# Optimization experiments

Measured on AMD Instinct MI355X. Metric: run time of the kernel, lower is better.

The kernel has to match this reference:

```python
import jax, jax.numpy as jnp
import numpy as np

IN_FEAT = 3 * 32 * 32  # channels*height*width
HID = 1024
CLASSES = 10
EPS = 1e-5


def binarize(w):
    # Deterministic BinaryConnect: sign(w) in {-1, +1} (sign(0) -> +1)
    return jnp.where(w >= 0, 1.0, -1.0).astype(w.dtype)


def batchnorm(h, gamma, beta):
    # training-mode BatchNorm1d: biased batch stats over batch axis
    mean = jnp.mean(h, axis=0)
    var = jnp.var(h, axis=0)
    return gamma * (h - mean) * jax.lax.rsqrt(var + EPS) + beta


def setup_inputs() -> dict:
    key = jax.random.key(0)
    ks = jax.random.split(key, 6)
    x = jax.random.normal(ks[0], (8192, 3, 32, 32), dtype=jnp.float32)
    # latent real-valued weights, torch Linear layout [out, in], kaiming-ish scale
    W1 = jax.random.normal(ks[1], (HID, IN_FEAT), dtype=jnp.float32) * (1.0 / np.sqrt(IN_FEAT))
    W2 = jax.random.normal(ks[2], (HID, HID), dtype=jnp.float32) * (1.0 / np.sqrt(HID))
    W3 = jax.random.normal(ks[3], (HID, HID), dtype=jnp.float32) * (1.0 / np.sqrt(HID))
    W4 = jax.random.normal(ks[4], (CLASSES, HID), dtype=jnp.float32) * (1.0 / np.sqrt(HID))
    g1 = jnp.ones((HID,), jnp.float32); b1 = jnp.zeros((HID,), jnp.float32)
    g2 = jnp.ones((HID,), jnp.float32); b2 = jnp.zeros((HID,), jnp.float32)
    g3 = jnp.ones((HID,), jnp.float32); b3 = jnp.zeros((HID,), jnp.float32)
    return {"x": x, "W1": W1, "W2": W2, "W3": W3, "W4": W4,
            "g1": g1, "b1": b1, "g2": g2, "b2": b2, "g3": g3, "b3": b3}


def reference(x, W1, W2, W3, W4, g1, b1, g2, b2, g3, b3):
    h = x.reshape(-1, IN_FEAT)                       # [B, 3072]
    h = jax.nn.relu(h @ binarize(W1).T)              # [B, 1024]
    h = batchnorm(h, g1, b1)
    h = jax.nn.relu(h @ binarize(W2).T)
    h = batchnorm(h, g2, b2)
    h = jax.nn.relu(h @ binarize(W3).T)
    h = batchnorm(h, g3, b3)
    return h @ binarize(W4).T                        # [B, classes]
```

## Files before the change

### kernel.cpp

```cpp
#include <hip/hip_runtime.h>
#include <stdint.h>

typedef unsigned short u16;
typedef __attribute__((ext_vector_type(8))) unsigned short ushort8;
typedef __attribute__((ext_vector_type(4))) unsigned short ushort4v;
typedef __attribute__((ext_vector_type(8))) __bf16 bf16x8;
typedef __attribute__((ext_vector_type(4))) float f32x4;

__device__ __forceinline__ u16 f2bf(float f) {
    union { float f; unsigned int u; } v; v.f = f;
    unsigned int r = v.u + 0x7FFFu + ((v.u >> 16) & 1u);
    return (u16)(r >> 16);
}
__device__ __forceinline__ float bf2f(u16 b) {
    union { unsigned int u; float f; } v; v.u = ((unsigned int)b) << 16;
    return v.f;
}

typedef __attribute__((address_space(1))) const uint32_t* gptr_t;
typedef __attribute__((address_space(3))) uint32_t* lptr_t;
__device__ __forceinline__ void async_copy16(const void* g, void* l) {
    __builtin_amdgcn_global_load_lds((gptr_t)g, (lptr_t)l, 16, 0, 0);
}


__global__ __launch_bounds__(256) void f32_to_bf16_kernel(
    const float* __restrict__ in, u16* __restrict__ out, int n8)
{
    int i = blockIdx.x * 256 + threadIdx.x;
    if (i >= n8) return;
    const float4* p = (const float4*)(in + (size_t)i * 8);
    float4 x0 = p[0], x1 = p[1];
    ushort8 o;
    o[0] = f2bf(x0.x); o[1] = f2bf(x0.y); o[2] = f2bf(x0.z); o[3] = f2bf(x0.w);
    o[4] = f2bf(x1.x); o[5] = f2bf(x1.y); o[6] = f2bf(x1.z); o[7] = f2bf(x1.w);
    *(ushort8*)(out + (size_t)i * 8) = o;
}

__global__ __launch_bounds__(256) void binarize_kernel(
    const float* __restrict__ in, u16* __restrict__ out, int n8)
{
    int i = blockIdx.x * 256 + threadIdx.x;
    if (i >= n8) return;
    const float4* p = (const float4*)(in + (size_t)i * 8);
    float4 x0 = p[0], x1 = p[1];
    ushort8 o;
    o[0] = x0.x >= 0.f ? 0x3F80 : 0xBF80;
    o[1] = x0.y >= 0.f ? 0x3F80 : 0xBF80;
    o[2] = x0.z >= 0.f ? 0x3F80 : 0xBF80;
    o[3] = x0.w >= 0.f ? 0x3F80 : 0xBF80;
    o[4] = x1.x >= 0.f ? 0x3F80 : 0xBF80;
    o[5] = x1.y >= 0.f ? 0x3F80 : 0xBF80;
    o[6] = x1.z >= 0.f ? 0x3F80 : 0xBF80;
    o[7] = x1.w >= 0.f ? 0x3F80 : 0xBF80;
    *(ushort8*)(out + (size_t)i * 8) = o;
}

__global__ __launch_bounds__(256) void build_w4t(
    const float* __restrict__ W4, u16* __restrict__ W4T)
{
    int idx = blockIdx.x * 256 + threadIdx.x;
    int k = idx >> 4, c = idx & 15;
    u16 v = 0;
    if (c < 10) v = (W4[(size_t)c * 1024 + k] >= 0.f) ? 0x3F80 : 0xBF80;
    W4T[idx] = v;
}

__global__ __launch_bounds__(256) void rescale_w(
    const float* __restrict__ W, const float* __restrict__ ss,
    u16* __restrict__ Wp, float* __restrict__ bias)
{
    const int lane = threadIdx.x & 63;
    const int wid  = threadIdx.x >> 6;
    const int r    = blockIdx.x * 4 + wid;
    float bsum = 0.f;
    #pragma unroll
    for (int k0 = 0; k0 < 1024; k0 += 256) {
        int k = k0 + lane * 4;
        float4 w  = *(const float4*)(W + (size_t)r * 1024 + k);
        float4 sc = *(const float4*)(ss + k);
        float4 sh = *(const float4*)(ss + 1024 + k);
        ushort4v o;
        o[0] = f2bf(w.x >= 0.f ? sc.x : -sc.x);
        o[1] = f2bf(w.y >= 0.f ? sc.y : -sc.y);
        o[2] = f2bf(w.z >= 0.f ? sc.z : -sc.z);
        o[3] = f2bf(w.w >= 0.f ? sc.w : -sc.w);
        bsum += (w.x >= 0.f ? sh.x : -sh.x) + (w.y >= 0.f ? sh.y : -sh.y)
              + (w.z >= 0.f ? sh.z : -sh.z) + (w.w >= 0.f ? sh.w : -sh.w);
        *(ushort4v*)(Wp + (size_t)r * 1024 + k) = o;
    }
    #pragma unroll
    for (int off = 32; off; off >>= 1) bsum += __shfl_xor(bsum, off, 64);
    if (lane == 0) bias[r] = bsum;
}


__global__ __launch_bounds__(256) void gemm_fused(
    const u16* __restrict__ A, const u16* __restrict__ B,
    u16* __restrict__ H, const float* __restrict__ bias,
    float* __restrict__ partS, float* __restrict__ partS2,
    int M, int N, int K)
{
    __shared__ __align__(16) u16 As[2][128 * 64];
    __shared__ __align__(16) u16 Bs[2][128 * 64];

    const int tid  = threadIdx.x;
    const int wid  = tid >> 6;
    const int lane = tid & 63;
    const int lr   = lane & 15;
    const int hk   = lane >> 4;
    const int x7   = lr & 7;
    const int wr   = wid >> 1;
    const int wc   = wid & 1;
    const int row0 = blockIdx.x * 128;
    const int col0 = blockIdx.y * 128;

    const int s_r = tid >> 3;
    const int s_c = (((tid & 7) ^ (s_r & 7)) << 3);
    const u16* gA = A + (size_t)(row0 + s_r) * K + s_c;
    const u16* gB = B + (size_t)(col0 + s_r) * K + s_c;

    int a_base[4], b_base[4];
    #pragma unroll
    for (int i = 0; i < 4; ++i) a_base[i] = (wr * 64 + i * 16 + lr) * 64;
    #pragma unroll
    for (int j = 0; j < 4; ++j) b_base[j] = (wc * 64 + j * 16 + lr) * 64;
    const int xs0 = ((hk)     ^ x7) << 3;
    const int xs1 = ((hk + 4) ^ x7) << 3;

    f32x4 acc[4][4];
    #pragma unroll
    for (int i = 0; i < 4; ++i)
        #pragma unroll
        for (int j = 0; j < 4; ++j)
            acc[i][j] = (f32x4){0.f, 0.f, 0.f, 0.f};

    const int NT = K >> 6;

    auto STAGE = [&](int buf, int t) {
        const u16* pa = gA + (size_t)t * 64;
        const u16* pb = gB + (size_t)t * 64;
        #pragma unroll
        for (int i = 0; i < 4; ++i)
            async_copy16(pa + (size_t)i * 32 * K, &As[buf][i * 2048 + wid * 512]);
        #pragma unroll
        for (int i = 0; i < 4; ++i)
            async_copy16(pb + (size_t)i * 32 * K, &Bs[buf][i * 2048 + wid * 512]);
    };

    STAGE(0, 0);
    STAGE(1, 1);

    for (int t = 0; t < NT; ++t) {
        const int buf = t & 1;
        if (t + 1 < NT) asm volatile("s_waitcnt vmcnt(8)" ::: "memory");
        else            asm volatile("s_waitcnt vmcnt(0)" ::: "memory");
        __builtin_amdgcn_s_barrier();

        bf16x8 af[4][2], bg[4][2];
        #pragma unroll
        for (int i = 0; i < 4; ++i) {
            af[i][0] = *(const bf16x8*)&As[buf][a_base[i] + xs0];
            af[i][1] = *(const bf16x8*)&As[buf][a_base[i] + xs1];
        }
        #pragma unroll
        for (int j = 0; j < 4; ++j) {
            bg[j][0] = *(const bf16x8*)&Bs[buf][b_base[j] + xs0];
            bg[j][1] = *(const bf16x8*)&Bs[buf][b_base[j] + xs1];
        }
        asm volatile("s_waitcnt lgkmcnt(0)" ::: "memory");
        __builtin_amdgcn_sched_barrier(0);
        __builtin_amdgcn_s_barrier();

        if (t + 2 < NT) STAGE(buf, t + 2);

        __builtin_amdgcn_s_setprio(1);
        #pragma unroll
        for (int kk = 0; kk < 2; ++kk)
            #pragma unroll
            for (int i = 0; i < 4; ++i)
                #pragma unroll
                for (int j = 0; j < 4; ++j)
                    acc[i][j] = __builtin_amdgcn_mfma_f32_16x16x32_bf16(
                        af[i][kk], bg[j][kk], acc[i][j], 0, 0, 0);
        __builtin_amdgcn_s_setprio(0);
    }

    const int er = hk * 4;
    #pragma unroll
    for (int j = 0; j < 4; ++j) {
        const int c = col0 + wc * 64 + j * 16 + lr;
        const float bj = bias ? bias[c] : 0.f;
        float s = 0.f, s2 = 0.f;
        #pragma unroll
        for (int i = 0; i < 4; ++i) {
            const int r = row0 + wr * 64 + i * 16 + er;
            #pragma unroll
            for (int b2 = 0; b2 < 4; ++b2) {
                float x = acc[i][j][b2] + bj;
                x = x > 0.f ? x : 0.f;
                s += x; s2 += x * x;
                H[(size_t)(r + b2) * N + c] = f2bf(x);
            }
        }
        s  += __shfl_xor(s, 16, 64);  s  += __shfl_xor(s, 32, 64);
        s2 += __shfl_xor(s2, 16, 64); s2 += __shfl_xor(s2, 32, 64);
        if (hk == 0) {
            const int p = blockIdx.x * 2 + wr;
            partS [(size_t)p * 1024 + c] = s;
            partS2[(size_t)p * 1024 + c] = s2;
        }
    }
}


__global__ __launch_bounds__(256) void bn_finalize(
    const float* __restrict__ partS, const float* __restrict__ partS2,
    const float* __restrict__ gamma, const float* __restrict__ beta,
    float* __restrict__ ss)
{
    int c = blockIdx.x * 256 + threadIdx.x;
    float s = 0.f, s2 = 0.f;
    for (int i = 0; i < 128; ++i) {
        s  += partS [(size_t)i * 1024 + c];
        s2 += partS2[(size_t)i * 1024 + c];
    }
    float mean = s * (1.0f / 8192.0f);
    float var  = fmaxf(s2 * (1.0f / 8192.0f) - mean * mean, 0.f);
    float sc   = gamma[c] * rsqrtf(var + 1e-5f);
    ss[c]        = sc;
    ss[1024 + c] = beta[c] - mean * sc;
}


__global__ __launch_bounds__(256) void head_kernel(
    const u16* __restrict__ H, const u16* __restrict__ W4T,
    const float* __restrict__ ss, float* __restrict__ out)
{
    const int lane = threadIdx.x & 63;
    const int wid  = threadIdx.x >> 6;
    const int r    = blockIdx.x * 4 + wid;

    float acc[10];
    #pragma unroll
    for (int c = 0; c < 10; c++) acc[c] = 0.f;

    #pragma unroll
    for (int j = 0; j < 16; ++j) {
        int k = j * 64 + lane;
        float a = fmaf(bf2f(H[(size_t)r * 1024 + k]), ss[k], ss[1024 + k]);
        ushort8 w0 = *(const ushort8*)(W4T + (size_t)k * 16);
        acc[0] += a * bf2f(w0[0]); acc[1] += a * bf2f(w0[1]);
        acc[2] += a * bf2f(w0[2]); acc[3] += a * bf2f(w0[3]);
        acc[4] += a * bf2f(w0[4]); acc[5] += a * bf2f(w0[5]);
        acc[6] += a * bf2f(w0[6]); acc[7] += a * bf2f(w0[7]);
        u16 w8 = W4T[(size_t)k * 16 + 8];
        u16 w9 = W4T[(size_t)k * 16 + 9];
        acc[8] += a * bf2f(w8);    acc[9] += a * bf2f(w9);
    }
    #pragma unroll
    for (int c = 0; c < 10; c++) {
        float s = acc[c];
        #pragma unroll
        for (int off = 32; off > 0; off >>= 1) s += __shfl_xor(s, off, 64);
        acc[c] = s;
    }
    if (lane == 0) {
        #pragma unroll
        for (int c = 0; c < 10; c++) out[(size_t)r * 10 + c] = acc[c];
    }
}


extern "C" void kernel_launch(void* const* d_in, const int* in_sizes, int n_in,
                              void* d_out, int out_size, void* d_ws, size_t ws_size,
                              hipStream_t stream) {
    const float* x  = (const float*)d_in[0];
    const float* W1 = (const float*)d_in[1];
    const float* W2 = (const float*)d_in[2];
    const float* W3 = (const float*)d_in[3];
    const float* W4 = (const float*)d_in[4];
    const float* g1 = (const float*)d_in[5];
    const float* b1 = (const float*)d_in[6];
    const float* g2 = (const float*)d_in[7];
    const float* b2 = (const float*)d_in[8];
    const float* g3 = (const float*)d_in[9];
    const float* b3 = (const float*)d_in[10];
    float* out = (float*)d_out;

    char* ws = (char*)d_ws;
    u16*   Xb    = (u16*)  (ws + 0);
    float* bias2 = (float*)(ws + 0);
    float* bias3 = (float*)(ws + 4096);
    u16*   Hb0   = (u16*)  (ws + 50331648);
    u16*   Hb1   = (u16*)  (ws + 67108864);
    u16*   W1b   = (u16*)  (ws + 83886080);
    u16*   W2p   = (u16*)  (ws + 90177536);
    u16*   W3p   = (u16*)  (ws + 92274688);
    u16*   W4T   = (u16*)  (ws + 94371840);
    float* partS = (float*)(ws + 94404608);
    float* partS2= (float*)(ws + 94928896);
    float* ss    = (float*)(ws + 95453184);

    f32_to_bf16_kernel<<<12288, 256, 0, stream>>>(x, Xb, 3145728);
    binarize_kernel<<<1536, 256, 0, stream>>>(W1, W1b, 393216);
    build_w4t<<<64, 256, 0, stream>>>(W4, W4T);

    dim3 gemm_grid(64, 8);

    gemm_fused<<<gemm_grid, 256, 0, stream>>>(Xb, W1b, Hb0, nullptr, partS, partS2, 8192, 1024, 3072);
    bn_finalize<<<4, 256, 0, stream>>>(partS, partS2, g1, b1, ss);
    rescale_w<<<256, 256, 0, stream>>>(W2, ss, W2p, bias2);

    gemm_fused<<<gemm_grid, 256, 0, stream>>>(Hb0, W2p, Hb1, bias2, partS, partS2, 8192, 1024, 1024);
    bn_finalize<<<4, 256, 0, stream>>>(partS, partS2, g2, b2, ss);
    rescale_w<<<256, 256, 0, stream>>>(W3, ss, W3p, bias3);

    gemm_fused<<<gemm_grid, 256, 0, stream>>>(Hb1, W3p, Hb0, bias3, partS, partS2, 8192, 1024, 1024);
    bn_finalize<<<4, 256, 0, stream>>>(partS, partS2, g3, b3, ss);

    head_kernel<<<2048, 256, 0, stream>>>(Hb0, W4T, ss, out);
}
```

Baseline: 191.1 us.

## Fuse fp32-to-bf16 input conversion into first-layer GEMM A-tile loading

Removes the standalone kernel that converted the 8192x3072 fp32 input to bf16. The first-layer GEMM now loads fp32 A tiles into registers, converts them to bf16 and writes them to swizzled LDS, while B still uses async global-to-LDS copies. The A loads run three tiles ahead of use. This drops a full write and re-read of the bf16 activation buffer, but every block now reads fp32 A directly (twice the bytes per tile, re-read across the 8 column blocks), and the register-staged path adds VGPR pressure and VALU conversion work inside the main loop.

```diff
diff --git a/kernel.cpp b/kernel.cpp
--- a/kernel.cpp
+++ b/kernel.cpp
@@ -5,6 +5,7 @@
 typedef __attribute__((ext_vector_type(8))) unsigned short ushort8;
 typedef __attribute__((ext_vector_type(4))) unsigned short ushort4v;
 typedef __attribute__((ext_vector_type(8))) __bf16 bf16x8;
+typedef __attribute__((ext_vector_type(4))) __bf16 bf16x4;
 typedef __attribute__((ext_vector_type(4))) float f32x4;
 
 __device__ __forceinline__ u16 f2bf(float f) {
@@ -23,19 +24,6 @@
     __builtin_amdgcn_global_load_lds((gptr_t)g, (lptr_t)l, 16, 0, 0);
 }
 
-
-__global__ __launch_bounds__(256) void f32_to_bf16_kernel(
-    const float* __restrict__ in, u16* __restrict__ out, int n8)
-{
-    int i = blockIdx.x * 256 + threadIdx.x;
-    if (i >= n8) return;
-    const float4* p = (const float4*)(in + (size_t)i * 8);
-    float4 x0 = p[0], x1 = p[1];
-    ushort8 o;
-    o[0] = f2bf(x0.x); o[1] = f2bf(x0.y); o[2] = f2bf(x0.z); o[3] = f2bf(x0.w);
-    o[4] = f2bf(x1.x); o[5] = f2bf(x1.y); o[6] = f2bf(x1.z); o[7] = f2bf(x1.w);
-    *(ushort8*)(out + (size_t)i * 8) = o;
-}
 
 __global__ __launch_bounds__(256) void binarize_kernel(
     const float* __restrict__ in, u16* __restrict__ out, int n8)
@@ -95,9 +83,9 @@
 }
 
 
-__global__ __launch_bounds__(256) void gemm_fused(
-    const u16* __restrict__ A, const u16* __restrict__ B,
-    u16* __restrict__ H, const float* __restrict__ bias,
+__global__ __launch_bounds__(256) void gemm1_f32a(
+    const float* __restrict__ A, const u16* __restrict__ B,
+    u16* __restrict__ H,
     float* __restrict__ partS, float* __restrict__ partS2,
     int M, int N, int K)
 {
@@ -117,8 +105,14 @@
 
     const int s_r = tid >> 3;
     const int s_c = (((tid & 7) ^ (s_r & 7)) << 3);
-    const u16* gA = A + (size_t)(row0 + s_r) * K + s_c;
     const u16* gB = B + (size_t)(col0 + s_r) * K + s_c;
+
+    const int a_r = tid >> 4;
+    const int a_c = (tid & 15) * 4;
+    const float* gA = A + (size_t)(row0 + a_r) * K + a_c;
+    const int a_c8 = (tid & 15) >> 1;
+    const int a_cw = (tid & 1) * 4;
+    float4 areg[8];
 
     int a_base[4], b_base[4];
     #pragma unroll
@@ -137,23 +131,41 @@
 
     const int NT = K >> 6;
 
-    auto STAGE = [&](int buf, int t) {
-        const u16* pa = gA + (size_t)t * 64;
+    auto LOADA = [&](int t) {
+        const float* p = gA + (size_t)t * 64;
+        #pragma unroll
+        for (int i = 0; i < 8; ++i)
+            areg[i] = *(const float4*)(p + (size_t)i * 16 * K);
+    };
+    auto WRITEA = [&](int buf) {
+        #pragma unroll
+        for (int i = 0; i < 8; ++i) {
+            int row = i * 16 + a_r;
+            u16* dst = &As[buf][row * 64 + ((a_c8 ^ (row & 7)) << 3) + a_cw];
+            bf16x4 o = { (__bf16)areg[i].x, (__bf16)areg[i].y,
+                         (__bf16)areg[i].z, (__bf16)areg[i].w };
+            *(bf16x4*)dst = o;
+        }
+    };
+    auto STAGEB = [&](int buf, int t) {
         const u16* pb = gB + (size_t)t * 64;
-        #pragma unroll
-        for (int i = 0; i < 4; ++i)
-            async_copy16(pa + (size_t)i * 32 * K, &As[buf][i * 2048 + wid * 512]);
         #pragma unroll
         for (int i = 0; i < 4; ++i)
             async_copy16(pb + (size_t)i * 32 * K, &Bs[buf][i * 2048 + wid * 512]);
     };
 
-    STAGE(0, 0);
-    STAGE(1, 1);
+    LOADA(0);
+    WRITEA(0);
+    LOADA(1);
+    STAGEB(0, 0);
+    WRITEA(1);
+    LOADA(2);
+    STAGEB(1, 1);
+    asm volatile("s_waitcnt lgkmcnt(0)" ::: "memory");
 
     for (int t = 0; t < NT; ++t) {
         const int buf = t & 1;
-        if (t + 1 < NT) asm volatile("s_waitcnt vmcnt(8)" ::: "memory");
+        if (t + 1 < NT) asm volatile("s_waitcnt vmcnt(12)" ::: "memory");
         else            asm volatile("s_waitcnt vmcnt(0)" ::: "memory");
         __builtin_amdgcn_s_barrier();
 
@@ -172,7 +184,11 @@
         __builtin_amdgcn_sched_barrier(0);
         __builtin_amdgcn_s_barrier();
 
-        if (t + 2 < NT) STAGE(buf, t + 2);
+        WRITEA(buf);
+        const int ta = (t + 3 < NT) ? t + 3 : NT - 1;
+        LOADA(ta);
+        const int tb = (t + 2 < NT) ? t + 2 : NT - 1;
+        STAGEB(buf, tb);
 
         __builtin_amdgcn_s_setprio(1);
         #pragma unroll
@@ -190,7 +206,125 @@
     #pragma unroll
     for (int j = 0; j < 4; ++j) {
         const int c = col0 + wc * 64 + j * 16 + lr;
-        const float bj = bias ? bias[c] : 0.f;
+        float s = 0.f, s2 = 0.f;
+        #pragma unroll
+        for (int i = 0; i < 4; ++i) {
+            const int r = row0 + wr * 64 + i * 16 + er;
+            #pragma unroll
+            for (int b2 = 0; b2 < 4; ++b2) {
+                float x = acc[i][j][b2];
+                x = x > 0.f ? x : 0.f;
+                s += x; s2 += x * x;
+                H[(size_t)(r + b2) * N + c] = f2bf(x);
+            }
+        }
+        s  += __shfl_xor(s, 16, 64);  s  += __shfl_xor(s, 32, 64);
+        s2 += __shfl_xor(s2, 16, 64); s2 += __shfl_xor(s2, 32, 64);
+        if (hk == 0) {
+            const int p = blockIdx.x * 2 + wr;
+            partS [(size_t)p * 1024 + c] = s;
+            partS2[(size_t)p * 1024 + c] = s2;
+        }
+    }
+}
+
+
+__global__ __launch_bounds__(256) void gemm_fused(
+    const u16* __restrict__ A, const u16* __restrict__ B,
+    u16* __restrict__ H, const float* __restrict__ bias,
+    float* __restrict__ partS, float* __restrict__ partS2,
+    int M, int N, int K)
+{
+    __shared__ __align__(16) u16 As[2][128 * 64];
+    __shared__ __align__(16) u16 Bs[2][128 * 64];
+
+    const int tid  = threadIdx.x;
+    const int wid  = tid >> 6;
+    const int lane = tid & 63;
+    const int lr   = lane & 15;
+    const int hk   = lane >> 4;
+    const int x7   = lr & 7;
+    const int wr   = wid >> 1;
+    const int wc   = wid & 1;
+    const int row0 = blockIdx.x * 128;
+    const int col0 = blockIdx.y * 128;
+
+    const int s_r = tid >> 3;
+    const int s_c = (((tid & 7) ^ (s_r & 7)) << 3);
+    const u16* gA = A + (size_t)(row0 + s_r) * K + s_c;
+    const u16* gB = B + (size_t)(col0 + s_r) * K + s_c;
+
+    int a_base[4], b_base[4];
+    #pragma unroll
+    for (int i = 0; i < 4; ++i) a_base[i] = (wr * 64 + i * 16 + lr) * 64;
+    #pragma unroll
+    for (int j = 0; j < 4; ++j) b_base[j] = (wc * 64 + j * 16 + lr) * 64;
+    const int xs0 = ((hk)     ^ x7) << 3;
+    const int xs1 = ((hk + 4) ^ x7) << 3;
+
+    f32x4 acc[4][4];
+    #pragma unroll
+    for (int i = 0; i < 4; ++i)
+        #pragma unroll
+        for (int j = 0; j < 4; ++j)
+            acc[i][j] = (f32x4){0.f, 0.f, 0.f, 0.f};
+
+    const int NT = K >> 6;
+
+    auto STAGE = [&](int buf, int t) {
+        const u16* pa = gA + (size_t)t * 64;
+        const u16* pb = gB + (size_t)t * 64;
+        #pragma unroll
+        for (int i = 0; i < 4; ++i)
+            async_copy16(pa + (size_t)i * 32 * K, &As[buf][i * 2048 + wid * 512]);
+        #pragma unroll
+        for (int i = 0; i < 4; ++i)
+            async_copy16(pb + (size_t)i * 32 * K, &Bs[buf][i * 2048 + wid * 512]);
+    };
+
+    STAGE(0, 0);
+    STAGE(1, 1);
+
+    for (int t = 0; t < NT; ++t) {
+        const int buf = t & 1;
+        if (t + 1 < NT) asm volatile("s_waitcnt vmcnt(8)" ::: "memory");
+        else            asm volatile("s_waitcnt vmcnt(0)" ::: "memory");
+        __builtin_amdgcn_s_barrier();
+
+        bf16x8 af[4][2], bg[4][2];
+        #pragma unroll
+        for (int i = 0; i < 4; ++i) {
+            af[i][0] = *(const bf16x8*)&As[buf][a_base[i] + xs0];
+            af[i][1] = *(const bf16x8*)&As[buf][a_base[i] + xs1];
+        }
+        #pragma unroll
+        for (int j = 0; j < 4; ++j) {
+            bg[j][0] = *(const bf16x8*)&Bs[buf][b_base[j] + xs0];
+            bg[j][1] = *(const bf16x8*)&Bs[buf][b_base[j] + xs1];
+        }
+        asm volatile("s_waitcnt lgkmcnt(0)" ::: "memory");
+        __builtin_amdgcn_sched_barrier(0);
+        __builtin_amdgcn_s_barrier();
+
+        if (t + 2 < NT) STAGE(buf, t + 2);
+
+        __builtin_amdgcn_s_setprio(1);
+        #pragma unroll
+        for (int kk = 0; kk < 2; ++kk)
+            #pragma unroll
+            for (int i = 0; i < 4; ++i)
+                #pragma unroll
+                for (int j = 0; j < 4; ++j)
+                    acc[i][j] = __builtin_amdgcn_mfma_f32_16x16x32_bf16(
+                        af[i][kk], bg[j][kk], acc[i][j], 0, 0, 0);
+        __builtin_amdgcn_s_setprio(0);
+    }
+
+    const int er = hk * 4;
+    #pragma unroll
+    for (int j = 0; j < 4; ++j) {
+        const int c = col0 + wc * 64 + j * 16 + lr;
+        const float bj = bias[c];
         float s = 0.f, s2 = 0.f;
         #pragma unroll
         for (int i = 0; i < 4; ++i) {
@@ -289,26 +423,24 @@
     float* out = (float*)d_out;
 
     char* ws = (char*)d_ws;
-    u16*   Xb    = (u16*)  (ws + 0);
-    float* bias2 = (float*)(ws + 0);
-    float* bias3 = (float*)(ws + 4096);
-    u16*   Hb0   = (u16*)  (ws + 50331648);
-    u16*   Hb1   = (u16*)  (ws + 67108864);
-    u16*   W1b   = (u16*)  (ws + 83886080);
-    u16*   W2p   = (u16*)  (ws + 90177536);
-    u16*   W3p   = (u16*)  (ws + 92274688);
-    u16*   W4T   = (u16*)  (ws + 94371840);
-    float* partS = (float*)(ws + 94404608);
-    float* partS2= (float*)(ws + 94928896);
-    float* ss    = (float*)(ws + 95453184);
-
-    f32_to_bf16_kernel<<<12288, 256, 0, stream>>>(x, Xb, 3145728);
+    u16*   Hb0    = (u16*)  (ws + 0);
+    u16*   Hb1    = (u16*)  (ws + 16777216);
+    u16*   W1b    = (u16*)  (ws + 33554432);
+    u16*   W2p    = (u16*)  (ws + 39845888);
+    u16*   W3p    = (u16*)  (ws + 41943040);
+    u16*   W4T    = (u16*)  (ws + 44040192);
+    float* partS  = (float*)(ws + 44072960);
+    float* partS2 = (float*)(ws + 44597248);
+    float* ss     = (float*)(ws + 45121536);
+    float* bias2  = (float*)(ws + 45129728);
+    float* bias3  = (float*)(ws + 45133824);
+
     binarize_kernel<<<1536, 256, 0, stream>>>(W1, W1b, 393216);
     build_w4t<<<64, 256, 0, stream>>>(W4, W4T);
 
     dim3 gemm_grid(64, 8);
 
-    gemm_fused<<<gemm_grid, 256, 0, stream>>>(Xb, W1b, Hb0, nullptr, partS, partS2, 8192, 1024, 3072);
+    gemm1_f32a<<<gemm_grid, 256, 0, stream>>>(x, W1b, Hb0, partS, partS2, 8192, 1024, 3072);
     bn_finalize<<<4, 256, 0, stream>>>(partS, partS2, g1, b1, ss);
     rescale_w<<<256, 256, 0, stream>>>(W2, ss, W2p, bias2);
 
```

Measured after the change: 197.1 us. 1.03x slower.
